# Optimization experiments

Hardware: AMD Instinct MI355X
Metric: run time of the kernel (lower is better)

Reference implementation:

```python
import jax, jax.numpy as jnp
import numpy as np
import math

EMBED = 256
NH = 8            # num_heads
HD = EMBED // NH  # head_dim = 32
LEVELS = 4
P = 4             # points per level
SUMP = LEVELS * P # 16
OFFSET_SCALE = 0.5
SPATIAL = ((80, 80), (40, 40), (20, 20), (10, 10))  # (H, W) per level
BS, LQ = 4, 4096
LV = sum(h * w for h, w in SPATIAL)  # 8500


def _offset_bias():
    # replicates _reset_parameters grid init for sampling_offsets.bias
    thetas = np.arange(NH, dtype=np.float32) * (2.0 * math.pi / NH)
    grid = np.stack([np.cos(thetas), np.sin(thetas)], -1)  # [NH,2]
    grid = grid / np.abs(grid).max(-1, keepdims=True)
    grid = np.tile(grid.reshape(NH, 1, 2), (1, SUMP, 1))   # [NH,SUMP,2]
    scaling = np.concatenate([np.arange(1, P + 1) for _ in range(LEVELS)]).reshape(1, SUMP, 1)
    grid = grid * scaling
    return jnp.asarray(grid.reshape(-1), dtype=jnp.float32)  # [NH*SUMP*2]


def setup_inputs() -> dict:
    key = jax.random.key(0)
    ks = jax.random.split(key, 8)
    xavier = lambda k, fi, fo: jax.random.uniform(k, (fi, fo), jnp.float32,
                                                  -math.sqrt(6.0 / (fi + fo)), math.sqrt(6.0 / (fi + fo)))
    return {
        "query": jax.random.normal(ks[0], (BS, LQ, EMBED), jnp.float32),
        "reference_points": jax.random.uniform(ks[1], (BS, LQ, 1, 4), jnp.float32),
        "value": jax.random.normal(ks[2], (BS, LV, EMBED), jnp.float32),
        # sampling_offsets: weight is zero-init in torch; use small random so offsets depend on query
        "W_off": jax.random.normal(ks[3], (EMBED, NH * SUMP * 2), jnp.float32) * 0.01,
        "b_off": _offset_bias(),
        "W_attn": jax.random.normal(ks[4], (EMBED, NH * SUMP), jnp.float32) * 0.01,
        "b_attn": jnp.zeros((NH * SUMP,), jnp.float32),
        "W_v": xavier(ks[5], EMBED, EMBED),
        "b_v": jnp.zeros((EMBED,), jnp.float32),
        "W_o": xavier(ks[6], EMBED, EMBED),
        "b_o": jnp.zeros((EMBED,), jnp.float32),
    }


def _bilinear_sample(v_l, loc, Hl, Wl):
    """grid_sample (bilinear, zero padding, align_corners=False) on one level.
    v_l: [bs, NH, Hl*Wl, HD]; loc: [bs, Lq, NH, P, 2] in [0,1] (x=width, y=height).
    Returns [bs, Lq, NH, P, HD]."""
    bs, lq, nh, p, _ = loc.shape
    x = loc[..., 0] * Wl - 0.5
    y = loc[..., 1] * Hl - 0.5
    x0 = jnp.floor(x)
    y0 = jnp.floor(y)
    lx, ly = x - x0, y - y0
    x0i = x0.astype(jnp.int32)
    y0i = y0.astype(jnp.int32)

    def corner(xi, yi, w):
        valid = ((xi >= 0) & (xi < Wl) & (yi >= 0) & (yi < Hl)).astype(v_l.dtype)
        idx = jnp.clip(yi, 0, Hl - 1) * Wl + jnp.clip(xi, 0, Wl - 1)  # [bs,Lq,NH,P]
        idx = jnp.transpose(idx, (0, 2, 1, 3)).reshape(bs, nh, lq * p)
        g = jnp.take_along_axis(v_l, idx[..., None], axis=2)          # [bs,NH,Lq*P,HD]
        g = g.reshape(bs, nh, lq, p, HD).transpose(0, 2, 1, 3, 4)     # [bs,Lq,NH,P,HD]
        return g * (w * valid)[..., None]

    return (corner(x0i, y0i, (1 - lx) * (1 - ly))
            + corner(x0i + 1, y0i, lx * (1 - ly))
            + corner(x0i, y0i + 1, (1 - lx) * ly)
            + corner(x0i + 1, y0i + 1, lx * ly))


def reference(query, reference_points, value, W_off, b_off, W_attn, b_attn, W_v, b_v, W_o, b_o):
    bs, lq = query.shape[:2]
    lv = value.shape[1]

    v = (value @ W_v + b_v).reshape(bs, lv, NH, HD)

    off = (query @ W_off + b_off).reshape(bs, lq, NH, SUMP, 2)
    attn = jax.nn.softmax((query @ W_attn + b_attn).reshape(bs, lq, NH, SUMP), axis=-1)

    # reference_points last dim == 4 path (box refs)
    nps = jnp.full((SUMP, 1), 1.0 / P, dtype=query.dtype)  # num_points_scale
    loc = (reference_points[:, :, None, :, :2]
           + off * nps * reference_points[:, :, None, :, 2:] * OFFSET_SCALE)  # [bs,Lq,NH,SUMP,2]

    out = jnp.zeros((bs, lq, NH, HD), dtype=query.dtype)
    v_start, p_start = 0, 0
    for (Hl, Wl) in SPATIAL:
        n = Hl * Wl
        v_l = jnp.transpose(v[:, v_start:v_start + n], (0, 2, 1, 3))  # [bs,NH,n,HD]
        loc_l = loc[:, :, :, p_start:p_start + P]
        w_l = attn[:, :, :, p_start:p_start + P]
        sampled = _bilinear_sample(v_l, loc_l, Hl, Wl)                # [bs,Lq,NH,P,HD]
        out = out + jnp.einsum('blhpd,blhp->blhd', sampled, w_l)
        v_start += n
        p_start += P

    return out.reshape(bs, lq, EMBED) @ W_o + b_o
```

## Files before the change

### kernel.cpp

```cpp
#include <hip/hip_runtime.h>

#define NH 8
#define HD 32
#define SUMP 16
#define LQ 4096
#define BS 4
#define LV 8500
#define NQ (BS * LQ)
#define MV (BS * LV)

typedef float f32x4 __attribute__((ext_vector_type(4)));
typedef _Float16 f16x8 __attribute__((ext_vector_type(8)));

__global__ __launch_bounds__(256) void prep_kernel(
    const float* __restrict__ Wv, const float* __restrict__ Woff,
    const float* __restrict__ Wattn, const float* __restrict__ Wo,
    const float* __restrict__ boff, const float* __restrict__ battn,
    _Float16* __restrict__ WtVf, _Float16* __restrict__ WtOAf,
    _Float16* __restrict__ WtOf, float* __restrict__ biasOA)
{
    int g = blockIdx.x * 256 + threadIdx.x;
    int gl; _Float16* dst; int which;
    if (g < 65536)       { gl = g;          dst = WtVf;  which = 0; }
    else if (g < 163840) { gl = g - 65536;  dst = WtOAf; which = 1; }
    else                 { gl = g - 163840; dst = WtOf;  which = 2; }
    int e = gl & 7, m16 = (gl >> 3) & 15, q = (gl >> 7) & 3, C = (gl >> 9) & 7, T = gl >> 12;
    int n = T * 16 + m16, k = C * 32 + q * 8 + e;
    float w;
    if (which == 0)      w = Wv[k * 256 + n];
    else if (which == 1) w = (n < 256) ? Woff[k * 256 + n] : Wattn[k * 128 + (n - 256)];
    else                 w = Wo[k * 256 + n];
    dst[gl] = (_Float16)w;
    if (blockIdx.x == 0) biasOA[threadIdx.x] = boff[threadIdx.x];
    if (blockIdx.x == 1 && threadIdx.x < 128) biasOA[256 + threadIdx.x] = battn[threadIdx.x];
}

__device__ __forceinline__ f16x8 cvt8(const float4& lo, const float4& hi) {
    f16x8 r;
    r[0] = (_Float16)lo.x; r[1] = (_Float16)lo.y; r[2] = (_Float16)lo.z; r[3] = (_Float16)lo.w;
    r[4] = (_Float16)hi.x; r[5] = (_Float16)hi.y; r[6] = (_Float16)hi.z; r[7] = (_Float16)hi.w;
    return r;
}

template <int NI, bool V_MODE, bool A_F16>
__device__ __forceinline__ void chunk_gemm(
    const float* __restrict__ A32, const _Float16* __restrict__ A16,
    const _Float16* __restrict__ Bf, const float* __restrict__ bias,
    void* __restrict__ Cv, int M, int N, int mchunk, int ntbase,
    _Float16* __restrict__ As )
{
    const int t = threadIdx.x;
    const int wave = t >> 6, lane = t & 63;
    const int quad = lane >> 4, l16 = lane & 15;

    {
        const int srow = t >> 2, schunk = t & 3;
        int gr = mchunk * 64 + srow;
        if (gr > M - 1) gr = M - 1;
        if (A_F16) {
            const _Float16* src = A16 + (size_t)gr * 256 + schunk * 64;
            f16x8 hb[8];
            #pragma unroll
            for (int j = 0; j < 8; ++j) hb[j] = *(const f16x8*)(src + j * 8);
            #pragma unroll
            for (int j = 0; j < 8; ++j) {
                int slot = (schunk * 8 + j) ^ (srow & 7);
                *(f16x8*)(As + srow * 256 + slot * 8) = hb[j];
            }
        } else {
            const float* src = A32 + (size_t)gr * 256 + schunk * 64;
            float4 buf[16];
            #pragma unroll
            for (int j = 0; j < 16; ++j) buf[j] = *(const float4*)(src + j * 4);
            #pragma unroll
            for (int j = 0; j < 8; ++j) {
                f16x8 h = cvt8(buf[2 * j], buf[2 * j + 1]);
                int slot = (schunk * 8 + j) ^ (srow & 7);
                *(f16x8*)(As + srow * 256 + slot * 8) = h;
            }
        }
    }
    __syncthreads();

    const int ntile0 = ntbase + wave * NI;
    const _Float16* bp[NI];
    #pragma unroll
    for (int ni = 0; ni < NI; ++ni)
        bp[ni] = Bf + (size_t)(ntile0 + ni) * 4096 + lane * 8;

    f16x8 bcur[NI], bnxt[NI];
    f32x4 acc[4][NI] = {};
    #pragma unroll
    for (int ni = 0; ni < NI; ++ni) bcur[ni] = *(const f16x8*)(bp[ni]);

    #pragma unroll
    for (int k = 0; k < 8; ++k) {
        if (k < 7) {
            #pragma unroll
            for (int ni = 0; ni < NI; ++ni) bnxt[ni] = *(const f16x8*)(bp[ni] + (k + 1) * 512);
        }
        f16x8 af[4];
        #pragma unroll
        for (int mi = 0; mi < 4; ++mi) {
            int row = mi * 16 + l16;
            int slot = (quad + k * 4) ^ (row & 7);
            af[mi] = *(const f16x8*)(As + row * 256 + slot * 8);
        }
        #pragma unroll
        for (int mi = 0; mi < 4; ++mi)
            #pragma unroll
            for (int ni = 0; ni < NI; ++ni)
                acc[mi][ni] = __builtin_amdgcn_mfma_f32_16x16x32_f16(af[mi], bcur[ni], acc[mi][ni], 0, 0, 0);
        if (k < 7) {
            #pragma unroll
            for (int ni = 0; ni < NI; ++ni) bcur[ni] = bnxt[ni];
        }
    }

    if (V_MODE) {
        #pragma unroll
        for (int mi = 0; mi < 4; ++mi) {
            int mq = mchunk * 64 + mi * 16 + quad * 4;
            size_t rb[4]; int vld[4];
            #pragma unroll
            for (int r = 0; r < 4; ++r) {
                int m = mq + r;
                vld[r] = (m < M);
                int mm = vld[r] ? m : 0;
                int b = mm / LV; int pos = mm - b * LV;
                rb[r] = ((size_t)b * NH * LV + pos) * 32;
            }
            #pragma unroll
            for (int ni = 0; ni < NI; ++ni) {
                int n = (ntile0 + ni) * 16 + l16;
                float bv = bias[n];
                int h = n >> 5, d = n & 31;
                size_t ho = (size_t)h * (LV * 32) + d;
                #pragma unroll
                for (int r = 0; r < 4; ++r)
                    if (vld[r]) ((_Float16*)Cv)[rb[r] + ho] = (_Float16)(acc[mi][ni][r] + bv);
            }
        }
    } else {
        #pragma unroll
        for (int ni = 0; ni < NI; ++ni) {
            int n = (ntile0 + ni) * 16 + l16;
            float bv = bias[n];
            #pragma unroll
            for (int mi = 0; mi < 4; ++mi) {
                int mq = mchunk * 64 + mi * 16 + quad * 4;
                #pragma unroll
                for (int r = 0; r < 4; ++r)
                    ((float*)Cv)[(size_t)(mq + r) * N + n] = acc[mi][ni][r] + bv;
            }
        }
    }
}

__global__ __launch_bounds__(256) void gemm_dual_kernel(
    const float* __restrict__ value, const _Float16* __restrict__ WtVf,
    const float* __restrict__ b_v, _Float16* __restrict__ v_f16,
    const float* __restrict__ query, const _Float16* __restrict__ WtOAf,
    const float* __restrict__ biasOA, float* __restrict__ oa)
{
    __shared__ __align__(16) _Float16 As[64 * 256];
    int bid = blockIdx.x;
    if (bid < 532) {
        chunk_gemm<4, true, false>(value, nullptr, WtVf, b_v, v_f16, MV, 256,
                                   bid, 0, As);
    } else {
        int g = bid - 532;
        chunk_gemm<3, false, false>(query, nullptr, WtOAf, biasOA, oa, NQ, 384,
                                    g >> 1, (g & 1) * 12, As);
    }
}

__global__ __launch_bounds__(256) void gemm_o_kernel(
    const _Float16* __restrict__ mid, const _Float16* __restrict__ WtOf,
    const float* __restrict__ b_o, float* __restrict__ out)
{
    __shared__ __align__(16) _Float16 As[64 * 256];
    chunk_gemm<4, false, true>(nullptr, mid, WtOf, b_o, out, NQ, 256,
                               blockIdx.x, 0, As);
}

__global__ void sample_kernel(
    const _Float16* __restrict__ v,
    const float* __restrict__ oa,
    const float* __restrict__ refp,
    _Float16* __restrict__ mid)
{
    const int row0 = blockIdx.x * 2;
    const int t = threadIdx.x;
    const int wave = t >> 6, lane = t & 63;

    __shared__ __align__(16) int2   s_pk[16 * 17];
    __shared__ __align__(16) float4 s_w4[16 * 17];
    __shared__ __align__(16) float  s_part[2 * 8 * 32];

    {
        int q = t >> 7, e = t & 127, h = e >> 4, p = e & 15, l = p >> 2;
        int row = row0 + q;
        float4 r4 = *(const float4*)(refp + (size_t)row * 4);
        float2 o2 = *(const float2*)(oa + (size_t)row * 384 + e * 2);
        float raw = oa[(size_t)row * 384 + 256 + e];

        float mx = raw;
        #pragma unroll
        for (int d = 8; d >= 1; d >>= 1) mx = fmaxf(mx, __shfl_xor(mx, d, 16));
        float ex = __expf(raw - mx);
        float sm = ex;
        #pragma unroll
        for (int d = 8; d >= 1; d >>= 1) sm += __shfl_xor(sm, d, 16);
        float w = ex * __builtin_amdgcn_rcpf(sm);

        int Wl = 80 >> l;
        int vst = (l == 0) ? 0 : (l == 1) ? 6400 : (l == 2) ? 8000 : 8400;
        float x = (r4.x + o2.x * 0.125f * r4.z) * Wl - 0.5f;
        float y = (r4.y + o2.y * 0.125f * r4.w) * Wl - 0.5f;
        float x0f = floorf(x), y0f = floorf(y);
        float lx = x - x0f, ly = y - y0f;
        int x0 = (int)x0f, y0 = (int)y0f;
        int x1 = x0 + 1, y1 = y0 + 1;
        float mx0 = (x0 >= 0 && x0 < Wl) ? 1.f : 0.f;
        float mx1 = (x1 >= 0 && x1 < Wl) ? 1.f : 0.f;
        float my0 = (y0 >= 0 && y0 < Wl) ? 1.f : 0.f;
        float my1 = (y1 >= 0 && y1 < Wl) ? 1.f : 0.f;
        int cx0 = min(max(x0, 0), Wl - 1), cx1 = min(max(x1, 0), Wl - 1);
        int cy0 = min(max(y0, 0), Wl - 1), cy1 = min(max(y1, 0), Wl - 1);
        int2 r_pk;
        float4 r_w4;
        r_pk.x = (vst + cy0 * Wl + cx0) * 64;
        r_pk.y = ((cx1 - cx0) * 64) | (((cy1 - cy0) * Wl * 64) << 16);
        r_w4.x = w * (1.f - lx) * (1.f - ly) * mx0 * my0;
        r_w4.y = w * lx * (1.f - ly) * mx1 * my0;
        r_w4.z = w * (1.f - lx) * ly * mx0 * my1;
        r_w4.w = w * lx * ly * mx1 * my1;
        int s = (q * 8 + h) * 17 + p;
        s_pk[s] = r_pk; s_w4[s] = r_w4;
    }
    __syncthreads();

    {
        const int q = wave >> 1, wp = wave & 1;
        const int pgl = lane >> 5, hh = (lane >> 2) & 7, dv2 = lane & 3;
        const int row = row0 + q;
        const int b = row >> 12;
        const char* vb = (const char*)v + ((size_t)(b * NH + hh) * LV) * 64 + dv2 * 16;

        int2 pk[4]; float4 w4[4];
        #pragma unroll
        for (int j = 0; j < 4; ++j) {
            int p = (wp * 2 + pgl) * 4 + j;
            int s = (q * 8 + hh) * 17 + p;
            pk[j] = s_pk[s]; w4[j] = s_w4[s];
        }
        f16x8 g0[4], g1[4], g2[4], g3[4];
        #pragma unroll
        for (int j = 0; j < 4; ++j) {
            int dx = pk[j].y & 0xffff, dy = pk[j].y >> 16;
            const char* base = vb + pk[j].x;
            g0[j] = *(const f16x8*)(base);
            g1[j] = *(const f16x8*)(base + dx);
            g2[j] = *(const f16x8*)(base + dy);
            g3[j] = *(const f16x8*)(base + dx + dy);
        }
        float acc8[8] = {};
        #pragma unroll
        for (int j = 0; j < 4; ++j)
            #pragma unroll
            for (int c = 0; c < 8; ++c)
                acc8[c] += w4[j].x * (float)g0[j][c] + w4[j].y * (float)g1[j][c]
                         + w4[j].z * (float)g2[j][c] + w4[j].w * (float)g3[j][c];

        #pragma unroll
        for (int c = 0; c < 8; ++c) acc8[c] += __shfl_xor(acc8[c], 32, 64);
        if (wp == 1 && lane < 32) {
            #pragma unroll
            for (int c = 0; c < 8; ++c) s_part[q * 256 + c * 32 + lane] = acc8[c];
        }
        __syncthreads();
        if (wp == 0 && lane < 32) {
            f16x8 m8;
            #pragma unroll
            for (int c = 0; c < 8; ++c)
                m8[c] = (_Float16)(acc8[c] + s_part[q * 256 + c * 32 + lane]);
            *(f16x8*)(mid + (size_t)row * 256 + hh * 32 + dv2 * 8) = m8;
        }
    }
}

extern "C" void kernel_launch(void* const* d_in, const int* in_sizes, int n_in,
                              void* d_out, int out_size, void* d_ws, size_t ws_size,
                              hipStream_t stream) {
    const float* query  = (const float*)d_in[0];
    const float* refp   = (const float*)d_in[1];
    const float* value  = (const float*)d_in[2];
    const float* W_off  = (const float*)d_in[3];
    const float* b_off  = (const float*)d_in[4];
    const float* W_attn = (const float*)d_in[5];
    const float* b_attn = (const float*)d_in[6];
    const float* W_v    = (const float*)d_in[7];
    const float* b_v    = (const float*)d_in[8];
    const float* W_o    = (const float*)d_in[9];
    const float* b_o    = (const float*)d_in[10];

    char* ws = (char*)d_ws;
    _Float16* v_f16  = (_Float16*)(ws + 0);
    float*    oa_f32 = (float*)(ws + 17408000);
    _Float16* mid    = (_Float16*)(ws + 42573824);
    _Float16* WtVf   = (_Float16*)(ws + 50962432);
    _Float16* WtOAf  = (_Float16*)(ws + 51093504);
    _Float16* WtOf   = (_Float16*)(ws + 51290112);
    float*    biasOA = (float*)(ws + 51421184);

    prep_kernel<<<896, 256, 0, stream>>>(W_v, W_off, W_attn, W_o, b_off, b_attn,
                                         WtVf, WtOAf, WtOf, biasOA);
    gemm_dual_kernel<<<1044, 256, 0, stream>>>(
        value, WtVf, b_v, v_f16, query, WtOAf, biasOA, oa_f32);
    sample_kernel<<<NQ / 2, 256, 0, stream>>>(v_f16, oa_f32, refp, mid);
    gemm_o_kernel<<<256, 256, 0, stream>>>(mid, WtOf, b_o, (float*)d_out);
}
```

Before: 178.4 us.

## Remap sample blocks to single (batch, head) per XCD for L2 locality

The sampling kernel now gives each block 16 query rows of a single (batch, head) pair instead of 2 rows across all 8 heads. Block indices are swizzled so that each of the 8 XCDs handles 4 fixed (batch, head) slices, which keeps each XCD's gathered value data (about 544 KB per head slice in fp16) resident in its own L2. The aim is to cut L2 misses and cross-die traffic on the random bilinear gathers. In exchange, the oa/refp reads become strided per head, and the stores to mid now write 64-byte fragments per row instead of full rows.

After: 169.0 us. 1.06x faster.

```diff
diff --git a/kernel.cpp b/kernel.cpp
--- a/kernel.cpp
+++ b/kernel.cpp
@@ -190,7 +190,13 @@
     const float* __restrict__ refp,
     _Float16* __restrict__ mid)
 {
-    const int row0 = blockIdx.x * 2;
+    const int blk = blockIdx.x;
+    const int xcd = blk & 7, j = blk >> 3;
+    const int bh = xcd * 4 + (j & 3);
+    const int chunk = j >> 2;
+    const int b = bh >> 3, h = bh & 7;
+    const int rowG0 = b * LQ + chunk * 16;
+
     const int t = threadIdx.x;
     const int wave = t >> 6, lane = t & 63;
 
@@ -199,11 +205,11 @@
     __shared__ __align__(16) float  s_part[2 * 8 * 32];
 
     {
-        int q = t >> 7, e = t & 127, h = e >> 4, p = e & 15, l = p >> 2;
-        int row = row0 + q;
+        int task = t >> 4, p = t & 15, l = p >> 2;
+        int row = rowG0 + task;
         float4 r4 = *(const float4*)(refp + (size_t)row * 4);
-        float2 o2 = *(const float2*)(oa + (size_t)row * 384 + e * 2);
-        float raw = oa[(size_t)row * 384 + 256 + e];
+        float2 o2 = *(const float2*)(oa + (size_t)row * 384 + (h * 16 + p) * 2);
+        float raw = oa[(size_t)row * 384 + 256 + h * 16 + p];
 
         float mx = raw;
         #pragma unroll
@@ -236,56 +242,56 @@
         r_w4.y = w * lx * (1.f - ly) * mx1 * my0;
         r_w4.z = w * (1.f - lx) * ly * mx0 * my1;
         r_w4.w = w * lx * ly * mx1 * my1;
-        int s = (q * 8 + h) * 17 + p;
+        int s = task * 17 + p;
         s_pk[s] = r_pk; s_w4[s] = r_w4;
     }
     __syncthreads();
 
     {
-        const int q = wave >> 1, wp = wave & 1;
-        const int pgl = lane >> 5, hh = (lane >> 2) & 7, dv2 = lane & 3;
-        const int row = row0 + q;
-        const int b = row >> 12;
-        const char* vb = (const char*)v + ((size_t)(b * NH + hh) * LV) * 64 + dv2 * 16;
+        const int wg = wave >> 1, wp = wave & 1;
+        const int pgl = lane >> 5, tk = (lane >> 2) & 7, dv2 = lane & 3;
+        const int task = wg * 8 + tk;
+        const int row = rowG0 + task;
+        const char* vb = (const char*)v + ((size_t)(b * NH + h) * LV) * 64 + dv2 * 16;
 
         int2 pk[4]; float4 w4[4];
         #pragma unroll
-        for (int j = 0; j < 4; ++j) {
-            int p = (wp * 2 + pgl) * 4 + j;
-            int s = (q * 8 + hh) * 17 + p;
-            pk[j] = s_pk[s]; w4[j] = s_w4[s];
+        for (int jj = 0; jj < 4; ++jj) {
+            int p = (wp * 2 + pgl) * 4 + jj;
+            int s = task * 17 + p;
+            pk[jj] = s_pk[s]; w4[jj] = s_w4[s];
         }
         f16x8 g0[4], g1[4], g2[4], g3[4];
         #pragma unroll
-        for (int j = 0; j < 4; ++j) {
-            int dx = pk[j].y & 0xffff, dy = pk[j].y >> 16;
-            const char* base = vb + pk[j].x;
-            g0[j] = *(const f16x8*)(base);
-            g1[j] = *(const f16x8*)(base + dx);
-            g2[j] = *(const f16x8*)(base + dy);
-            g3[j] = *(const f16x8*)(base + dx + dy);
+        for (int jj = 0; jj < 4; ++jj) {
+            int dx = pk[jj].y & 0xffff, dy = pk[jj].y >> 16;
+            const char* base = vb + pk[jj].x;
+            g0[jj] = *(const f16x8*)(base);
+            g1[jj] = *(const f16x8*)(base + dx);
+            g2[jj] = *(const f16x8*)(base + dy);
+            g3[jj] = *(const f16x8*)(base + dx + dy);
         }
         float acc8[8] = {};
         #pragma unroll
-        for (int j = 0; j < 4; ++j)
+        for (int jj = 0; jj < 4; ++jj)
             #pragma unroll
             for (int c = 0; c < 8; ++c)
-                acc8[c] += w4[j].x * (float)g0[j][c] + w4[j].y * (float)g1[j][c]
-                         + w4[j].z * (float)g2[j][c] + w4[j].w * (float)g3[j][c];
+                acc8[c] += w4[jj].x * (float)g0[jj][c] + w4[jj].y * (float)g1[jj][c]
+                         + w4[jj].z * (float)g2[jj][c] + w4[jj].w * (float)g3[jj][c];
 
         #pragma unroll
         for (int c = 0; c < 8; ++c) acc8[c] += __shfl_xor(acc8[c], 32, 64);
         if (wp == 1 && lane < 32) {
             #pragma unroll
-            for (int c = 0; c < 8; ++c) s_part[q * 256 + c * 32 + lane] = acc8[c];
+            for (int c = 0; c < 8; ++c) s_part[wg * 256 + c * 32 + lane] = acc8[c];
         }
         __syncthreads();
         if (wp == 0 && lane < 32) {
             f16x8 m8;
             #pragma unroll
             for (int c = 0; c < 8; ++c)
-                m8[c] = (_Float16)(acc8[c] + s_part[q * 256 + c * 32 + lane]);
-            *(f16x8*)(mid + (size_t)row * 256 + hh * 32 + dv2 * 8) = m8;
+                m8[c] = (_Float16)(acc8[c] + s_part[wg * 256 + c * 32 + lane]);
+            *(f16x8*)(mid + (size_t)row * 256 + h * 32 + dv2 * 8) = m8;
         }
     }
 }
@@ -318,6 +324,6 @@
                                          WtVf, WtOAf, WtOf, biasOA);
     gemm_dual_kernel<<<1044, 256, 0, stream>>>(
         value, WtVf, b_v, v_f16, query, WtOAf, biasOA, oa_f32);
-    sample_kernel<<<NQ / 2, 256, 0, stream>>>(v_f16, oa_f32, refp, mid);
+    sample_kernel<<<8192, 256, 0, stream>>>(v_f16, oa_f32, refp, mid);
     gemm_o_kernel<<<256, 256, 0, stream>>>(mid, WtOf, b_o, (float*)d_out);
 }
```
